# Kernel tuning notes

Measured on AMD Instinct MI355X. Metric: run time of the kernel, lower is better.

Reference implementation:

```python
import jax, jax.numpy as jnp
import numpy as np

# ---- layer config (yolov3, layer_no=2) ----
STRIDE = 8
N_CLASSES = 80
IGNORE_TH = 0.7
ANCHORS_PX = np.array([[10,13],[16,30],[33,23],[30,61],[62,45],[59,119],[116,90],[156,198],[373,326]], np.float32)
ALL_ANCHORS = ANCHORS_PX / STRIDE          # [9,2] in grid units
ANCHOR_ID_LO, ANCHOR_ID_HI = 0, 2          # anchor_mask[2] = [0,1,2]
ANCHORS = ALL_ANCHORS[ANCHOR_ID_LO:ANCHOR_ID_HI+1]  # [3,2]
NA = 3
NC = N_CLASSES + 5

B, IN_CH, NG, NBOX = 16, 256, 76, 50


def _safe_log(p):
    # emulate torch BCE's log clamp at -100; eps stops 0*inf -> nan
    return jnp.maximum(jnp.log(jnp.maximum(p, 1e-12)), -100.0)


def _bce_sum(p, t, w=None):
    l = -(t * _safe_log(p) + (1.0 - t) * _safe_log(1.0 - p))
    if w is not None:
        l = l * w
    return l.sum()


def setup_inputs() -> dict:
    key = jax.random.key(0)
    k1, k2, k3, k4, k5 = jax.random.split(key, 5)
    xin = jax.random.normal(k1, (B, IN_CH, NG, NG), jnp.float32)
    cls = jax.random.randint(k2, (B, NBOX, 1), 0, N_CLASSES).astype(jnp.float32)
    cxy = jax.random.uniform(k3, (B, NBOX, 2), jnp.float32, 0.02, 0.98)
    wh = jax.random.uniform(k4, (B, NBOX, 2), jnp.float32, 0.02, 0.40)
    labels = jnp.concatenate([cls, cxy, wh], axis=-1)  # [B,N,5]
    W = jax.random.normal(k5, (NA * NC, IN_CH), jnp.float32) * 0.02  # 1x1 conv
    b = jnp.zeros((NA * NC,), jnp.float32)
    return {"xin": xin, "labels": labels, "W": W, "b": b}


def _yolo_loss(xin, labels, W, b):
    nB, _, nG, _ = xin.shape
    anchors = jnp.asarray(ANCHORS, xin.dtype)          # [3,2]
    all_anchors = jnp.asarray(ALL_ANCHORS, xin.dtype)  # [9,2]

    # 1x1 conv -> [B, A, G, G, C]
    x = jnp.einsum('bchw,oc->bohw', xin, W) + b[None, :, None, None]
    x = x.reshape(nB, NA, NC, nG, nG).transpose(0, 1, 3, 4, 2)

    xy = jax.nn.sigmoid(x[..., :2])
    wh = x[..., 2:4]
    conf_cls = jax.nn.sigmoid(x[..., 4:])  # [B,A,G,G,1+ncls]

    gy, gx = jnp.meshgrid(jnp.arange(nG, dtype=x.dtype), jnp.arange(nG, dtype=x.dtype), indexing='ij')
    pred_boxes = jnp.stack([
        xy[..., 0] + gx,
        xy[..., 1] + gy,
        jnp.exp(wh[..., 0]) * anchors[:, 0][None, :, None, None],
        jnp.exp(wh[..., 1]) * anchors[:, 1][None, :, None, None]], axis=-1)  # [B,A,G,G,4]

    # ---- ground truth ----
    valid = labels.sum(-1) > 0                     # [B,N]
    gt_cls = labels[..., 0].astype(jnp.int32)
    gt = labels[..., 1:] * nG                      # [B,N,4] cx,cy,w,h in grid units
    gt_x, gt_y, gt_w, gt_h = gt[..., 0], gt[..., 1], gt[..., 2], gt[..., 3]
    gi = jnp.floor(gt_x).astype(jnp.int32)
    gj = jnp.floor(gt_y).astype(jnp.int32)

    # best anchor per gt: wh-IoU vs all 9 anchors (centered at origin)
    inter_a = jnp.minimum(gt_w[..., None], all_anchors[:, 0]) * jnp.minimum(gt_h[..., None], all_anchors[:, 1])
    union_a = gt_w[..., None] * gt_h[..., None] + all_anchors[:, 0] * all_anchors[:, 1] - inter_a
    best = jnp.argmax(inter_a / union_a, axis=-1)  # [B,N]
    in_mask = (best >= ANCHOR_ID_LO) & (best <= ANCHOR_ID_HI)
    a = jnp.where(in_mask, best % 3, -1)           # [B,N]

    # all-pairs IoU: pred boxes vs gt boxes (ignore mask)
    pb = pred_boxes.reshape(nB, -1, 4)             # [B,M,4], M = A*G*G
    pa_area = pb[..., 2] * pb[..., 3]
    gt_area = gt_w * gt_h
    tl = jnp.maximum(pb[:, :, None, :2] - pb[:, :, None, 2:] / 2, gt[:, None, :, :2] - gt[:, None, :, 2:] / 2)
    br = jnp.minimum(pb[:, :, None, :2] + pb[:, :, None, 2:] / 2, gt[:, None, :, :2] + gt[:, None, :, 2:] / 2)
    inter = jnp.prod(br - tl, -1) * jnp.all(tl < br, -1)
    iou = inter / (pa_area[:, :, None] + gt_area[:, None, :] - inter)
    iou = jnp.where(valid[:, None, :], iou, 0.0)
    best_iou = iou.max(-1)                         # [B,M]
    has_boxes = valid.any(-1)
    obj_mask = jnp.where(has_boxes[:, None], best_iou <= IGNORE_TH, True).reshape(nB, NA, nG, nG)

    # ---- scatter target assignment ----
    assign = valid & (a >= 0)
    a_safe = jnp.clip(a, 0, NA - 1)
    aw = anchors[a_safe, 0]
    ah = anchors[a_safe, 1]
    tvec = jnp.concatenate([
        (gt_x - jnp.floor(gt_x))[..., None],
        (gt_y - jnp.floor(gt_y))[..., None],
        jnp.log(gt_w / aw + 1e-16)[..., None],
        jnp.log(gt_h / ah + 1e-16)[..., None],
        jnp.ones_like(gt_x)[..., None],
        jax.nn.one_hot(gt_cls, N_CLASSES, dtype=x.dtype)], axis=-1)  # [B,N,NC]
    sval = 2.0 - gt_w * gt_h / (nG * nG)

    bf = jnp.broadcast_to(jnp.arange(nB)[:, None], a.shape).reshape(-1)
    af = jnp.where(assign, a_safe, NA).reshape(-1)  # NA is OOB -> dropped
    jf = gj.reshape(-1)
    if_ = gi.reshape(-1)

    target = jnp.zeros((nB, NA, nG, nG, NC), x.dtype).at[bf, af, jf, if_].set(tvec.reshape(-1, NC), mode='drop')
    scale = jnp.zeros((nB, NA, nG, nG), x.dtype).at[bf, af, jf, if_].set(sval.reshape(-1), mode='drop')
    obj_mask = obj_mask.at[bf, af, jf, if_].set(True, mode='drop')
    noobj = jnp.zeros((nB, NA, nG, nG), bool).at[bf, af, jf, if_].set(True, mode='drop')

    # ---- losses ----
    nm = noobj.astype(x.dtype)[..., None]
    p_obj = conf_cls[..., 0] * obj_mask
    t_obj = target[..., 4] * obj_mask
    p_xy = xy * nm
    t_xy = target[..., :2] * nm
    p_wh = wh * nm
    t_wh = target[..., 2:4] * nm
    p_cls = conf_cls[..., 1:] * nm
    t_cls = target[..., 5:] * nm
    sc = scale[..., None]

    loss_xy = _bce_sum(p_xy, t_xy, sc)
    rs = jnp.sqrt(sc)
    loss_wh = 0.5 * jnp.sum((p_wh * rs - t_wh * rs) ** 2)
    loss_obj = _bce_sum(p_obj, t_obj)
    loss_cls = _bce_sum(p_cls, t_cls)
    loss = loss_xy + loss_wh + loss_obj + loss_cls
    return jnp.stack([loss, loss_xy, loss_wh, loss_obj, loss_cls])


def reference(xin, labels, W, b):
    return _yolo_loss(xin, labels, W, b)
```

## Files before the change

kernel.cpp:

```cpp
#include <hip/hip_runtime.h>
#include <math.h>

#define NB    16
#define NAg   3
#define NCg   85
#define NCLS  80
#define NGg   76
#define NSp   (NGg*NGg)
#define NBOX  50
#define INCH  256
#define SPB   256

#define ACC_OFF  0
#define HAS_OFF  32
#define WT_OFF   128
#define GB_OFF   (WT_OFF + 16384)
#define GA_OFF   (GB_OFF + 25600)
#define GI_OFF   (GA_OFF + 25600)

__device__ __constant__ float c_AW[9] = {1.25f,2.0f,4.125f,3.75f,7.75f,7.375f,14.5f,19.5f,46.625f};
__device__ __constant__ float c_AH[9] = {1.625f,3.75f,2.875f,7.625f,5.625f,14.875f,11.25f,24.75f,40.75f};

__device__ __forceinline__ float safe_log(float p) {
    return fmaxf(logf(fmaxf(p, 1e-12f)), -100.0f);
}
__device__ __forceinline__ float sigm(float x) {
    return 1.0f / (1.0f + expf(-x));
}

__global__ __launch_bounds__(256) void k_labels(
    const float* __restrict__ labels, const float* __restrict__ W,
    float* __restrict__ Wt, float* __restrict__ gbox, float* __restrict__ gaux,
    int* __restrict__ gint, int* __restrict__ hasAny, float* __restrict__ acc)
{
    const int b = blockIdx.x, tid = threadIdx.x;
    const int t = b * 256 + tid;

    {
        const int c = t >> 4, f = t & 15;
        Wt[t] = (f < 15) ? W[((f / 5) * NCg + (f % 5)) * INCH + c] : 0.f;
    }
    if (b == 0 && tid < 8) acc[tid] = 0.f;

    int valid = 0;
    if (tid < NBOX) {
        const int bt = b * NBOX + tid;
        const float* L = labels + (size_t)bt * 5;
        const float l0 = L[0], l1 = L[1], l2 = L[2], l3 = L[3], l4 = L[4];
        valid = (l0 + l1 + l2 + l3 + l4) > 0.f;

        const float gx = l1 * NGg, gy = l2 * NGg, gw = l3 * NGg, gh = l4 * NGg;

        int best = 0; float brr = -1.f;
#pragma unroll
        for (int k = 0; k < 9; k++) {
            float inter = fminf(gw, c_AW[k]) * fminf(gh, c_AH[k]);
            float uni   = gw*gh + c_AW[k]*c_AH[k] - inter;
            float r     = inter / uni;
            if (r > brr) { brr = r; best = k; }
        }
        const int a = (best <= 2) ? best : -1;
        const int assign = valid && (a >= 0);
        const int a_safe = a < 0 ? 0 : (a > 2 ? 2 : a);

        const int gi = (int)floorf(gx), gj = (int)floorf(gy);
        const int inb = (gi >= 0) && (gi < NGg) && (gj >= 0) && (gj < NGg);
        const int cell = (assign && inb) ? (a * NSp + gj * NGg + gi) : -1;

        float* gb = gbox + (size_t)bt * 8;
        gb[0] = gx - gw * 0.5f;
        gb[1] = gy - gh * 0.5f;
        gb[2] = gx + gw * 0.5f;
        gb[3] = gy + gh * 0.5f;
        gb[4] = valid ? gw * gh : -1.f;
        gb[5] = __int_as_float(cell);

        float* ga = gaux + (size_t)bt * 8;
        ga[0] = gx - floorf(gx);
        ga[1] = gy - floorf(gy);
        ga[2] = logf(gw / c_AW[a_safe] + 1e-16f);
        ga[3] = logf(gh / c_AH[a_safe] + 1e-16f);
        ga[4] = 2.f - gw * gh / (float)NSp;

        gint[bt*2 + 0] = cell;
        gint[bt*2 + 1] = (int)l0;
    }
    if (tid < 64) {
        const unsigned long long m = __ballot(valid != 0);
        if (tid == 0) hasAny[b] = (m != 0ULL) ? 1 : 0;
    }
}

__global__ __launch_bounds__(256) void k_main(
    const float* __restrict__ xin, const float* __restrict__ Wt,
    const float* __restrict__ bias, const float* __restrict__ gbox,
    const int* __restrict__ hasAny, float* __restrict__ acc)
{
    __shared__ float part[4][15][SPB];
    __shared__ float wred[4];

    const int b   = blockIdx.y;
    const int tid = threadIdx.x;
    const int w   = tid >> 6, l = tid & 63;
    const int wu  = __builtin_amdgcn_readfirstlane(w);
    const int pb  = blockIdx.x * SPB;

    float4 ac[15];
#pragma unroll
    for (int f = 0; f < 15; ++f) ac[f] = make_float4(0.f,0.f,0.f,0.f);

    const float* xp = xin + ((size_t)b * INCH + (wu << 6)) * NSp + pb + 4*l;
    const float* wp = Wt + ((wu << 6) << 4);

    if (pb + SPB <= NSp) {
        for (int c0 = 0; c0 < 64; c0 += 8) {
            float4 v[8];
#pragma unroll
            for (int k = 0; k < 8; ++k)
                v[k] = *(const float4*)(xp + (size_t)(c0 + k) * NSp);
#pragma unroll
            for (int k = 0; k < 8; ++k) {
                const float* wr = wp + ((c0 + k) << 4);
#pragma unroll
                for (int f = 0; f < 15; ++f) {
                    const float wv = wr[f];
                    ac[f].x += wv * v[k].x;  ac[f].y += wv * v[k].y;
                    ac[f].z += wv * v[k].z;  ac[f].w += wv * v[k].w;
                }
            }
        }
    } else {
        const bool lv = (pb + 4*l) < NSp;
        const float4 z = make_float4(0.f,0.f,0.f,0.f);
        for (int c0 = 0; c0 < 64; c0 += 8) {
            float4 v[8];
#pragma unroll
            for (int k = 0; k < 8; ++k)
                v[k] = lv ? *(const float4*)(xp + (size_t)(c0 + k) * NSp) : z;
#pragma unroll
            for (int k = 0; k < 8; ++k) {
                const float* wr = wp + ((c0 + k) << 4);
#pragma unroll
                for (int f = 0; f < 15; ++f) {
                    const float wv = wr[f];
                    ac[f].x += wv * v[k].x;  ac[f].y += wv * v[k].y;
                    ac[f].z += wv * v[k].z;  ac[f].w += wv * v[k].w;
                }
            }
        }
    }

#pragma unroll
    for (int f = 0; f < 15; ++f)
        *(float4*)&part[w][f][4*l] = ac[f];
    __syncthreads();

    float lsum = 0.f;
    const int p = pb + tid;
    if (p < NSp) {
        float xv[15];
#pragma unroll
        for (int f = 0; f < 15; ++f)
            xv[f] = part[0][f][tid] + part[1][f][tid]
                  + part[2][f][tid] + part[3][f][tid];

        const int sy = p / NGg;
        const int sx = p - sy * NGg;
        const float gxf = (float)sx, gyf = (float)sy;

        float pbx0[3], pby0[3], pbx1[3], pby1[3], pa[3], cf[3];
#pragma unroll
        for (int a = 0; a < 3; ++a) {
            const float px = sigm(xv[a*5+0] + bias[a*NCg+0]) + gxf;
            const float py = sigm(xv[a*5+1] + bias[a*NCg+1]) + gyf;
            const float pw = expf(xv[a*5+2] + bias[a*NCg+2]) * c_AW[a];
            const float ph = expf(xv[a*5+3] + bias[a*NCg+3]) * c_AH[a];
            cf[a]   = sigm(xv[a*5+4] + bias[a*NCg+4]);
            pbx0[a] = px - pw * 0.5f;  pby0[a] = py - ph * 0.5f;
            pbx1[a] = px + pw * 0.5f;  pby1[a] = py + ph * 0.5f;
            pa[a]   = pw * ph;
        }

        int mask = 0;
        const float* gb = gbox + (size_t)b * NBOX * 8;
        for (int n = 0; n < NBOX; ++n) {
            const float bx0 = gb[n*8+0], by0 = gb[n*8+1];
            const float bx1 = gb[n*8+2], by1 = gb[n*8+3];
            const float gar = gb[n*8+4];
            const int cell  = __float_as_int(gb[n*8+5]);
            const int d = cell - p;
            if (d == 0)       mask |= 8;
            if (d == NSp)     mask |= 16;
            if (d == 2*NSp)   mask |= 32;
            if (gar >= 0.f) {
#pragma unroll
                for (int a = 0; a < 3; ++a) {
                    const float tlx = fmaxf(pbx0[a], bx0);
                    const float tly = fmaxf(pby0[a], by0);
                    const float brx = fminf(pbx1[a], bx1);
                    const float bry = fminf(pby1[a], by1);
                    const float dx = brx - tlx, dy = bry - tly;
                    const float inter = (dx > 0.f && dy > 0.f) ? dx * dy : 0.f;
                    if (inter > 0.7f * (pa[a] + gar - inter)) mask |= (1 << a);
                }
            }
        }

        const bool hasB = hasAny[b] != 0;
#pragma unroll
        for (int a = 0; a < 3; ++a) {
            const bool ex = (mask & (1 << a)) != 0;
            const bool as = (mask & (8 << a)) != 0;
            const bool maskpre = hasB ? (!ex) : true;
            if (maskpre || as) {
                const float c = cf[a];
                lsum += as ? -safe_log(c) : -safe_log(1.f - c);
            }
        }
    }

#pragma unroll
    for (int off = 32; off > 0; off >>= 1) lsum += __shfl_down(lsum, off);
    if (l == 0) wred[w] = lsum;
    __syncthreads();
    if (tid == 0) atomicAdd(&acc[2], wred[0] + wred[1] + wred[2] + wred[3]);
}

__global__ __launch_bounds__(256) void k_assigned(
    const float* __restrict__ xin, const float* __restrict__ W,
    const float* __restrict__ bias, const float* __restrict__ gaux,
    const int* __restrict__ gint, float* __restrict__ acc)
{
    const int t = blockIdx.x;
    const int b = t / NBOX, n = t % NBOX;
    const int tid = threadIdx.x;

    __shared__ int   scell[NBOX];
    __shared__ float4 col4[64];
    __shared__ float  xsh[NCg];
    __shared__ float  sacc[3];

    if (tid < NBOX) scell[tid] = gint[(b * NBOX + tid) * 2];
    __syncthreads();

    const int cell = scell[n];
    if (cell < 0) return;
    for (int n2 = n + 1; n2 < NBOX; ++n2)
        if (scell[n2] == cell) return;

    const int a = cell / NSp, s = cell % NSp;
    const int o0 = a * NCg;

    ((float*)col4)[tid] = xin[((size_t)b * INCH + tid) * NSp + s];
    if (tid < 3) sacc[tid] = 0.f;
    __syncthreads();

    const int wid = tid >> 6, lane = tid & 63;
    for (int o = wid; o < NCg; o += 4) {
        const float4 wv = *(const float4*)&W[(size_t)(o0 + o) * INCH + lane * 4];
        const float4 cv = col4[lane];
        float p = wv.x*cv.x + wv.y*cv.y + wv.z*cv.z + wv.w*cv.w;
        for (int off = 32; off; off >>= 1) p += __shfl_down(p, off);
        if (lane == 0) xsh[o] = p + bias[o0 + o];
    }
    __syncthreads();

    if (tid < NCg) {
        const float* ga = gaux + (size_t)t * 8;
        const float sval = ga[4];
        const int gcls = gint[t*2 + 1];
        float val = xsh[tid];
        float term; int slot;
        if (tid < 2) {
            float tgt = ga[tid];
            float p = sigm(val);
            term = -(tgt * safe_log(p) + (1.f - tgt) * safe_log(1.f - p)) * sval;
            slot = 0;
        } else if (tid < 4) {
            float tgt = ga[tid];
            float d = val - tgt;
            term = 0.5f * sval * d * d;
            slot = 1;
        } else if (tid == 4) {
            term = 0.f; slot = 2;
        } else {
            float tgt = ((tid - 5) == gcls) ? 1.f : 0.f;
            float p = sigm(val);
            term = -(tgt * safe_log(p) + (1.f - tgt) * safe_log(1.f - p));
            slot = 2;
        }
        atomicAdd(&sacc[slot], term);
    }
    __syncthreads();
    if (tid == 0) {
        atomicAdd(&acc[0], sacc[0]);
        atomicAdd(&acc[1], sacc[1]);
        atomicAdd(&acc[3], sacc[2]);
    }
}

__global__ void k_final(const float* __restrict__ acc, float* __restrict__ out)
{
    float xy = acc[0], wh = acc[1], ob = acc[2], cl = acc[3];
    out[0] = xy + wh + ob + cl;
    out[1] = xy; out[2] = wh; out[3] = ob; out[4] = cl;
}

extern "C" void kernel_launch(void* const* d_in, const int* in_sizes, int n_in,
                              void* d_out, int out_size, void* d_ws, size_t ws_size,
                              hipStream_t stream)
{
    const float* xin    = (const float*)d_in[0];
    const float* labels = (const float*)d_in[1];
    const float* W      = (const float*)d_in[2];
    const float* bias   = (const float*)d_in[3];

    char* ws = (char*)d_ws;
    float* acc    = (float*)(ws + ACC_OFF);
    int*   hasAny = (int*)  (ws + HAS_OFF);
    float* Wt     = (float*)(ws + WT_OFF);
    float* gbox   = (float*)(ws + GB_OFF);
    float* gaux   = (float*)(ws + GA_OFF);
    int*   gint   = (int*)  (ws + GI_OFF);
    float* out    = (float*)d_out;

    k_labels<<<16, 256, 0, stream>>>(labels, W, Wt, gbox, gaux, gint, hasAny, acc);

    k_main<<<dim3((NSp + SPB - 1) / SPB, NB), 256, 0, stream>>>(xin, Wt, bias, gbox, hasAny, acc);

    k_assigned<<<dim3(NB * NBOX), 256, 0, stream>>>(xin, W, bias, gaux, gint, acc);

    k_final<<<1, 1, 0, stream>>>(acc, out);
}
```

Baseline: 194.7 us.

## Merge main, assigned-cell and final kernels into one launch with last-block finish

Folds the per-cell objectness kernel, the assigned-box kernel and the final reduction kernel into a single launch. Extra blocks along x handle the assigned boxes, and a global done counter lets the last block write the output. This removes two kernel launches and their serialization gaps. In exchange it adds a shared-memory union, an atomic counter with a fence per block, and extra barriers on the assigned path.

Result: slower. 205.2 us (+5.4%).

```diff
diff --git a/kernel.cpp b/kernel.cpp
--- a/kernel.cpp
+++ b/kernel.cpp
@@ -10,9 +10,13 @@
 #define NBOX  50
 #define INCH  256
 #define SPB   256
+#define GBLK  ((NSp + SPB - 1) / SPB)
+#define GXDIM (GBLK + NBOX)
+#define TOTBLK (GXDIM * NB)
 
 #define ACC_OFF  0
 #define HAS_OFF  32
+#define DONE_OFF 96
 #define WT_OFF   128
 #define GB_OFF   (WT_OFF + 16384)
 #define GA_OFF   (GB_OFF + 25600)
@@ -31,7 +35,8 @@
 __global__ __launch_bounds__(256) void k_labels(
     const float* __restrict__ labels, const float* __restrict__ W,
     float* __restrict__ Wt, float* __restrict__ gbox, float* __restrict__ gaux,
-    int* __restrict__ gint, int* __restrict__ hasAny, float* __restrict__ acc)
+    int* __restrict__ gint, int* __restrict__ hasAny, float* __restrict__ acc,
+    int* __restrict__ done)
 {
     const int b = blockIdx.x, tid = threadIdx.x;
     const int t = b * 256 + tid;
@@ -40,7 +45,8 @@
         const int c = t >> 4, f = t & 15;
         Wt[t] = (f < 15) ? W[((f / 5) * NCg + (f % 5)) * INCH + c] : 0.f;
     }
-    if (b == 0 && tid < 8) acc[tid] = 0.f;
+    if (b == 0 && tid < 8)  acc[tid] = 0.f;
+    if (b == 0 && tid == 8) *done = 0;
 
     int valid = 0;
     if (tid < NBOX) {
@@ -91,219 +97,231 @@
     }
 }
 
-__global__ __launch_bounds__(256) void k_main(
+__global__ __launch_bounds__(256) void k_mega(
     const float* __restrict__ xin, const float* __restrict__ Wt,
-    const float* __restrict__ bias, const float* __restrict__ gbox,
-    const int* __restrict__ hasAny, float* __restrict__ acc)
+    const float* __restrict__ W, const float* __restrict__ bias,
+    const float* __restrict__ gbox, const float* __restrict__ gaux,
+    const int* __restrict__ gint, const int* __restrict__ hasAny,
+    float* __restrict__ acc, int* __restrict__ done, float* __restrict__ out)
 {
-    __shared__ float part[4][15][SPB];
-    __shared__ float wred[4];
-
+    __shared__ __align__(16) float smem[15364];
+
+    const int bx  = blockIdx.x;
     const int b   = blockIdx.y;
     const int tid = threadIdx.x;
-    const int w   = tid >> 6, l = tid & 63;
-    const int wu  = __builtin_amdgcn_readfirstlane(w);
-    const int pb  = blockIdx.x * SPB;
-
-    float4 ac[15];
-#pragma unroll
-    for (int f = 0; f < 15; ++f) ac[f] = make_float4(0.f,0.f,0.f,0.f);
-
-    const float* xp = xin + ((size_t)b * INCH + (wu << 6)) * NSp + pb + 4*l;
-    const float* wp = Wt + ((wu << 6) << 4);
-
-    if (pb + SPB <= NSp) {
-        for (int c0 = 0; c0 < 64; c0 += 8) {
-            float4 v[8];
-#pragma unroll
-            for (int k = 0; k < 8; ++k)
-                v[k] = *(const float4*)(xp + (size_t)(c0 + k) * NSp);
-#pragma unroll
-            for (int k = 0; k < 8; ++k) {
-                const float* wr = wp + ((c0 + k) << 4);
-#pragma unroll
-                for (int f = 0; f < 15; ++f) {
-                    const float wv = wr[f];
-                    ac[f].x += wv * v[k].x;  ac[f].y += wv * v[k].y;
-                    ac[f].z += wv * v[k].z;  ac[f].w += wv * v[k].w;
-                }
-            }
-        }
+
+    if (bx < GBLK) {
+        float (*part)[15][SPB] = (float (*)[15][SPB])smem;
+        float* wred = smem + 4 * 15 * SPB;
+
+        const int w  = tid >> 6, l = tid & 63;
+        const int wu = __builtin_amdgcn_readfirstlane(w);
+        const int pb = bx * SPB;
+
+        float4 ac[15];
+#pragma unroll
+        for (int f = 0; f < 15; ++f) ac[f] = make_float4(0.f,0.f,0.f,0.f);
+
+        const float* xp = xin + ((size_t)b * INCH + (wu << 6)) * NSp + pb + 4*l;
+        const float* wp = Wt + ((wu << 6) << 4);
+
+        if (pb + SPB <= NSp) {
+            for (int c0 = 0; c0 < 64; c0 += 8) {
+                float4 v[8];
+#pragma unroll
+                for (int k = 0; k < 8; ++k)
+                    v[k] = *(const float4*)(xp + (size_t)(c0 + k) * NSp);
+#pragma unroll
+                for (int k = 0; k < 8; ++k) {
+                    const float* wr = wp + ((c0 + k) << 4);
+#pragma unroll
+                    for (int f = 0; f < 15; ++f) {
+                        const float wv = wr[f];
+                        ac[f].x += wv * v[k].x;  ac[f].y += wv * v[k].y;
+                        ac[f].z += wv * v[k].z;  ac[f].w += wv * v[k].w;
+                    }
+                }
+            }
+        } else {
+            const bool lv = (pb + 4*l) < NSp;
+            const float4 z = make_float4(0.f,0.f,0.f,0.f);
+            for (int c0 = 0; c0 < 64; c0 += 8) {
+                float4 v[8];
+#pragma unroll
+                for (int k = 0; k < 8; ++k)
+                    v[k] = lv ? *(const float4*)(xp + (size_t)(c0 + k) * NSp) : z;
+#pragma unroll
+                for (int k = 0; k < 8; ++k) {
+                    const float* wr = wp + ((c0 + k) << 4);
+#pragma unroll
+                    for (int f = 0; f < 15; ++f) {
+                        const float wv = wr[f];
+                        ac[f].x += wv * v[k].x;  ac[f].y += wv * v[k].y;
+                        ac[f].z += wv * v[k].z;  ac[f].w += wv * v[k].w;
+                    }
+                }
+            }
+        }
+
+#pragma unroll
+        for (int f = 0; f < 15; ++f)
+            *(float4*)&part[w][f][4*l] = ac[f];
+        __syncthreads();
+
+        float lsum = 0.f;
+        const int p = pb + tid;
+        if (p < NSp) {
+            float xv[15];
+#pragma unroll
+            for (int f = 0; f < 15; ++f)
+                xv[f] = part[0][f][tid] + part[1][f][tid]
+                      + part[2][f][tid] + part[3][f][tid];
+
+            const int sy = p / NGg;
+            const int sx = p - sy * NGg;
+            const float gxf = (float)sx, gyf = (float)sy;
+
+            float pbx0[3], pby0[3], pbx1[3], pby1[3], pa[3], cf[3];
+#pragma unroll
+            for (int a = 0; a < 3; ++a) {
+                const float px = sigm(xv[a*5+0] + bias[a*NCg+0]) + gxf;
+                const float py = sigm(xv[a*5+1] + bias[a*NCg+1]) + gyf;
+                const float pw = expf(xv[a*5+2] + bias[a*NCg+2]) * c_AW[a];
+                const float ph = expf(xv[a*5+3] + bias[a*NCg+3]) * c_AH[a];
+                cf[a]   = sigm(xv[a*5+4] + bias[a*NCg+4]);
+                pbx0[a] = px - pw * 0.5f;  pby0[a] = py - ph * 0.5f;
+                pbx1[a] = px + pw * 0.5f;  pby1[a] = py + ph * 0.5f;
+                pa[a]   = pw * ph;
+            }
+
+            int mask = 0;
+            const float* gb = gbox + (size_t)b * NBOX * 8;
+            for (int n = 0; n < NBOX; ++n) {
+                const float bx0 = gb[n*8+0], by0 = gb[n*8+1];
+                const float bx1 = gb[n*8+2], by1 = gb[n*8+3];
+                const float gar = gb[n*8+4];
+                const int cell  = __float_as_int(gb[n*8+5]);
+                const int d = cell - p;
+                if (d == 0)       mask |= 8;
+                if (d == NSp)     mask |= 16;
+                if (d == 2*NSp)   mask |= 32;
+                if (gar >= 0.f) {
+#pragma unroll
+                    for (int a = 0; a < 3; ++a) {
+                        const float tlx = fmaxf(pbx0[a], bx0);
+                        const float tly = fmaxf(pby0[a], by0);
+                        const float brx = fminf(pbx1[a], bx1);
+                        const float bry = fminf(pby1[a], by1);
+                        const float dx = brx - tlx, dy = bry - tly;
+                        const float inter = (dx > 0.f && dy > 0.f) ? dx * dy : 0.f;
+                        if (inter > 0.7f * (pa[a] + gar - inter)) mask |= (1 << a);
+                    }
+                }
+            }
+
+            const bool hasB = hasAny[b] != 0;
+#pragma unroll
+            for (int a = 0; a < 3; ++a) {
+                const bool ex = (mask & (1 << a)) != 0;
+                const bool as = (mask & (8 << a)) != 0;
+                const bool maskpre = hasB ? (!ex) : true;
+                if (maskpre || as) {
+                    const float c = cf[a];
+                    lsum += as ? -safe_log(c) : -safe_log(1.f - c);
+                }
+            }
+        }
+
+#pragma unroll
+        for (int off = 32; off > 0; off >>= 1) lsum += __shfl_down(lsum, off);
+        if ((tid & 63) == 0) wred[tid >> 6] = lsum;
+        __syncthreads();
+        if (tid == 0) atomicAdd(&acc[2], wred[0] + wred[1] + wred[2] + wred[3]);
+
     } else {
-        const bool lv = (pb + 4*l) < NSp;
-        const float4 z = make_float4(0.f,0.f,0.f,0.f);
-        for (int c0 = 0; c0 < 64; c0 += 8) {
-            float4 v[8];
-#pragma unroll
-            for (int k = 0; k < 8; ++k)
-                v[k] = lv ? *(const float4*)(xp + (size_t)(c0 + k) * NSp) : z;
-#pragma unroll
-            for (int k = 0; k < 8; ++k) {
-                const float* wr = wp + ((c0 + k) << 4);
-#pragma unroll
-                for (int f = 0; f < 15; ++f) {
-                    const float wv = wr[f];
-                    ac[f].x += wv * v[k].x;  ac[f].y += wv * v[k].y;
-                    ac[f].z += wv * v[k].z;  ac[f].w += wv * v[k].w;
-                }
-            }
-        }
-    }
-
-#pragma unroll
-    for (int f = 0; f < 15; ++f)
-        *(float4*)&part[w][f][4*l] = ac[f];
-    __syncthreads();
-
-    float lsum = 0.f;
-    const int p = pb + tid;
-    if (p < NSp) {
-        float xv[15];
-#pragma unroll
-        for (int f = 0; f < 15; ++f)
-            xv[f] = part[0][f][tid] + part[1][f][tid]
-                  + part[2][f][tid] + part[3][f][tid];
-
-        const int sy = p / NGg;
-        const int sx = p - sy * NGg;
-        const float gxf = (float)sx, gyf = (float)sy;
-
-        float pbx0[3], pby0[3], pbx1[3], pby1[3], pa[3], cf[3];
-#pragma unroll
-        for (int a = 0; a < 3; ++a) {
-            const float px = sigm(xv[a*5+0] + bias[a*NCg+0]) + gxf;
-            const float py = sigm(xv[a*5+1] + bias[a*NCg+1]) + gyf;
-            const float pw = expf(xv[a*5+2] + bias[a*NCg+2]) * c_AW[a];
-            const float ph = expf(xv[a*5+3] + bias[a*NCg+3]) * c_AH[a];
-            cf[a]   = sigm(xv[a*5+4] + bias[a*NCg+4]);
-            pbx0[a] = px - pw * 0.5f;  pby0[a] = py - ph * 0.5f;
-            pbx1[a] = px + pw * 0.5f;  pby1[a] = py + ph * 0.5f;
-            pa[a]   = pw * ph;
-        }
-
-        int mask = 0;
-        const float* gb = gbox + (size_t)b * NBOX * 8;
-        for (int n = 0; n < NBOX; ++n) {
-            const float bx0 = gb[n*8+0], by0 = gb[n*8+1];
-            const float bx1 = gb[n*8+2], by1 = gb[n*8+3];
-            const float gar = gb[n*8+4];
-            const int cell  = __float_as_int(gb[n*8+5]);
-            const int d = cell - p;
-            if (d == 0)       mask |= 8;
-            if (d == NSp)     mask |= 16;
-            if (d == 2*NSp)   mask |= 32;
-            if (gar >= 0.f) {
-#pragma unroll
-                for (int a = 0; a < 3; ++a) {
-                    const float tlx = fmaxf(pbx0[a], bx0);
-                    const float tly = fmaxf(pby0[a], by0);
-                    const float brx = fminf(pbx1[a], bx1);
-                    const float bry = fminf(pby1[a], by1);
-                    const float dx = brx - tlx, dy = bry - tly;
-                    const float inter = (dx > 0.f && dy > 0.f) ? dx * dy : 0.f;
-                    if (inter > 0.7f * (pa[a] + gar - inter)) mask |= (1 << a);
-                }
-            }
-        }
-
-        const bool hasB = hasAny[b] != 0;
-#pragma unroll
-        for (int a = 0; a < 3; ++a) {
-            const bool ex = (mask & (1 << a)) != 0;
-            const bool as = (mask & (8 << a)) != 0;
-            const bool maskpre = hasB ? (!ex) : true;
-            if (maskpre || as) {
-                const float c = cf[a];
-                lsum += as ? -safe_log(c) : -safe_log(1.f - c);
-            }
-        }
-    }
-
-#pragma unroll
-    for (int off = 32; off > 0; off >>= 1) lsum += __shfl_down(lsum, off);
-    if (l == 0) wred[w] = lsum;
-    __syncthreads();
-    if (tid == 0) atomicAdd(&acc[2], wred[0] + wred[1] + wred[2] + wred[3]);
-}
-
-__global__ __launch_bounds__(256) void k_assigned(
-    const float* __restrict__ xin, const float* __restrict__ W,
-    const float* __restrict__ bias, const float* __restrict__ gaux,
-    const int* __restrict__ gint, float* __restrict__ acc)
-{
-    const int t = blockIdx.x;
-    const int b = t / NBOX, n = t % NBOX;
-    const int tid = threadIdx.x;
-
-    __shared__ int   scell[NBOX];
-    __shared__ float4 col4[64];
-    __shared__ float  xsh[NCg];
-    __shared__ float  sacc[3];
-
-    if (tid < NBOX) scell[tid] = gint[(b * NBOX + tid) * 2];
-    __syncthreads();
-
-    const int cell = scell[n];
-    if (cell < 0) return;
-    for (int n2 = n + 1; n2 < NBOX; ++n2)
-        if (scell[n2] == cell) return;
-
-    const int a = cell / NSp, s = cell % NSp;
-    const int o0 = a * NCg;
-
-    ((float*)col4)[tid] = xin[((size_t)b * INCH + tid) * NSp + s];
-    if (tid < 3) sacc[tid] = 0.f;
-    __syncthreads();
-
-    const int wid = tid >> 6, lane = tid & 63;
-    for (int o = wid; o < NCg; o += 4) {
-        const float4 wv = *(const float4*)&W[(size_t)(o0 + o) * INCH + lane * 4];
-        const float4 cv = col4[lane];
-        float p = wv.x*cv.x + wv.y*cv.y + wv.z*cv.z + wv.w*cv.w;
-        for (int off = 32; off; off >>= 1) p += __shfl_down(p, off);
-        if (lane == 0) xsh[o] = p + bias[o0 + o];
-    }
-    __syncthreads();
-
-    if (tid < NCg) {
-        const float* ga = gaux + (size_t)t * 8;
-        const float sval = ga[4];
-        const int gcls = gint[t*2 + 1];
-        float val = xsh[tid];
-        float term; int slot;
-        if (tid < 2) {
-            float tgt = ga[tid];
-            float p = sigm(val);
-            term = -(tgt * safe_log(p) + (1.f - tgt) * safe_log(1.f - p)) * sval;
-            slot = 0;
-        } else if (tid < 4) {
-            float tgt = ga[tid];
-            float d = val - tgt;
-            term = 0.5f * sval * d * d;
-            slot = 1;
-        } else if (tid == 4) {
-            term = 0.f; slot = 2;
-        } else {
-            float tgt = ((tid - 5) == gcls) ? 1.f : 0.f;
-            float p = sigm(val);
-            term = -(tgt * safe_log(p) + (1.f - tgt) * safe_log(1.f - p));
-            slot = 2;
-        }
-        atomicAdd(&sacc[slot], term);
-    }
+        int*    scell = (int*)smem;
+        float4* col4  = (float4*)(smem + 64);
+        float*  xsh   = smem + 64 + 256;
+        float*  sacc  = smem + 64 + 256 + 96;
+
+        const int n = bx - GBLK;
+        const int t = b * NBOX + n;
+
+        if (tid < NBOX) scell[tid] = gint[(b * NBOX + tid) * 2];
+        __syncthreads();
+
+        const int cell = scell[n];
+        bool win = (cell >= 0);
+        if (win)
+            for (int n2 = n + 1; n2 < NBOX; ++n2)
+                if (scell[n2] == cell) { win = false; break; }
+
+        if (win) {
+            const int a = cell / NSp, s = cell % NSp;
+            const int o0 = a * NCg;
+
+            ((float*)col4)[tid] = xin[((size_t)b * INCH + tid) * NSp + s];
+            if (tid < 3) sacc[tid] = 0.f;
+            __syncthreads();
+
+            const int wid = tid >> 6, lane = tid & 63;
+            for (int o = wid; o < NCg; o += 4) {
+                const float4 wv = *(const float4*)&W[(size_t)(o0 + o) * INCH + lane * 4];
+                const float4 cv = col4[lane];
+                float p = wv.x*cv.x + wv.y*cv.y + wv.z*cv.z + wv.w*cv.w;
+                for (int off = 32; off; off >>= 1) p += __shfl_down(p, off);
+                if (lane == 0) xsh[o] = p + bias[o0 + o];
+            }
+            __syncthreads();
+
+            if (tid < NCg) {
+                const float* ga = gaux + (size_t)t * 8;
+                const float sval = ga[4];
+                const int gcls = gint[t*2 + 1];
+                float val = xsh[tid];
+                float term; int slot;
+                if (tid < 2) {
+                    float tgt = ga[tid];
+                    float p = sigm(val);
+                    term = -(tgt * safe_log(p) + (1.f - tgt) * safe_log(1.f - p)) * sval;
+                    slot = 0;
+                } else if (tid < 4) {
+                    float tgt = ga[tid];
+                    float d = val - tgt;
+                    term = 0.5f * sval * d * d;
+                    slot = 1;
+                } else if (tid == 4) {
+                    term = 0.f; slot = 2;
+                } else {
+                    float tgt = ((tid - 5) == gcls) ? 1.f : 0.f;
+                    float p = sigm(val);
+                    term = -(tgt * safe_log(p) + (1.f - tgt) * safe_log(1.f - p));
+                    slot = 2;
+                }
+                atomicAdd(&sacc[slot], term);
+            }
+            __syncthreads();
+            if (tid == 0) {
+                atomicAdd(&acc[0], sacc[0]);
+                atomicAdd(&acc[1], sacc[1]);
+                atomicAdd(&acc[3], sacc[2]);
+            }
+        }
+    }
+
     __syncthreads();
     if (tid == 0) {
-        atomicAdd(&acc[0], sacc[0]);
-        atomicAdd(&acc[1], sacc[1]);
-        atomicAdd(&acc[3], sacc[2]);
-    }
-}
-
-__global__ void k_final(const float* __restrict__ acc, float* __restrict__ out)
-{
-    float xy = acc[0], wh = acc[1], ob = acc[2], cl = acc[3];
-    out[0] = xy + wh + ob + cl;
-    out[1] = xy; out[2] = wh; out[3] = ob; out[4] = cl;
+        __threadfence();
+        const int v = atomicAdd(done, 1);
+        if (v == TOTBLK - 1) {
+            const float xy = atomicAdd(&acc[0], 0.f);
+            const float wh = atomicAdd(&acc[1], 0.f);
+            const float ob = atomicAdd(&acc[2], 0.f);
+            const float cl = atomicAdd(&acc[3], 0.f);
+            out[0] = xy + wh + ob + cl;
+            out[1] = xy; out[2] = wh; out[3] = ob; out[4] = cl;
+        }
+    }
 }
 
 extern "C" void kernel_launch(void* const* d_in, const int* in_sizes, int n_in,
@@ -318,17 +336,15 @@
     char* ws = (char*)d_ws;
     float* acc    = (float*)(ws + ACC_OFF);
     int*   hasAny = (int*)  (ws + HAS_OFF);
+    int*   done   = (int*)  (ws + DONE_OFF);
     float* Wt     = (float*)(ws + WT_OFF);
     float* gbox   = (float*)(ws + GB_OFF);
     float* gaux   = (float*)(ws + GA_OFF);
     int*   gint   = (int*)  (ws + GI_OFF);
     float* out    = (float*)d_out;
 
-    k_labels<<<16, 256, 0, stream>>>(labels, W, Wt, gbox, gaux, gint, hasAny, acc);
-
-    k_main<<<dim3((NSp + SPB - 1) / SPB, NB), 256, 0, stream>>>(xin, Wt, bias, gbox, hasAny, acc);
-
-    k_assigned<<<dim3(NB * NBOX), 256, 0, stream>>>(xin, W, bias, gaux, gint, acc);
-
-    k_final<<<1, 1, 0, stream>>>(acc, out);
-}
+    k_labels<<<16, 256, 0, stream>>>(labels, W, Wt, gbox, gaux, gint, hasAny, acc, done);
+
+    k_mega<<<dim3(GXDIM, NB), 256, 0, stream>>>(xin, Wt, W, bias, gbox, gaux,
+                                                gint, hasAny, acc, done, out);
+}
```

## Give each thread four pixels over all channels and fold final reduction into last block

Applied to the files above, without the earlier changes.

k_main now has each thread accumulate all 256 input channels for four consecutive pixels and run the IoU/objectness loss on all four itself. This removes the per-wave channel split and its shared-memory partial-sum reduction and barrier. The separate k_final launch is replaced by a done-counter, so whichever block finishes last writes the output. k_assigned now runs before k_main. The grid shrinks to 6x16 blocks with a long serial channel loop per thread, which risks poor occupancy and latency hiding on a large GPU.

After: 313.6 us. 61.1% more time.

```diff
diff --git a/kernel.cpp b/kernel.cpp
--- a/kernel.cpp
+++ b/kernel.cpp
@@ -9,10 +9,13 @@
 #define NSp   (NGg*NGg)
 #define NBOX  50
 #define INCH  256
-#define SPB   256
+#define SPB   1024
+#define GBLK  ((NSp + SPB - 1) / SPB)
+#define TOTALL (GBLK * NB + NB * NBOX)
 
 #define ACC_OFF  0
 #define HAS_OFF  32
+#define DONE_OFF 96
 #define WT_OFF   128
 #define GB_OFF   (WT_OFF + 16384)
 #define GA_OFF   (GB_OFF + 25600)
@@ -31,7 +34,8 @@
 __global__ __launch_bounds__(256) void k_labels(
     const float* __restrict__ labels, const float* __restrict__ W,
     float* __restrict__ Wt, float* __restrict__ gbox, float* __restrict__ gaux,
-    int* __restrict__ gint, int* __restrict__ hasAny, float* __restrict__ acc)
+    int* __restrict__ gint, int* __restrict__ hasAny, float* __restrict__ acc,
+    int* __restrict__ done)
 {
     const int b = blockIdx.x, tid = threadIdx.x;
     const int t = b * 256 + tid;
@@ -40,7 +44,8 @@
         const int c = t >> 4, f = t & 15;
         Wt[t] = (f < 15) ? W[((f / 5) * NCg + (f % 5)) * INCH + c] : 0.f;
     }
-    if (b == 0 && tid < 8) acc[tid] = 0.f;
+    if (b == 0 && tid < 8)  acc[tid] = 0.f;
+    if (b == 0 && tid == 8) *done = 0;
 
     int valid = 0;
     if (tid < NBOX) {
@@ -91,130 +96,196 @@
     }
 }
 
+__global__ __launch_bounds__(256) void k_assigned(
+    const float* __restrict__ xin, const float* __restrict__ W,
+    const float* __restrict__ bias, const float* __restrict__ gaux,
+    const int* __restrict__ gint, float* __restrict__ acc,
+    int* __restrict__ done, float* __restrict__ out)
+{
+    const int t = blockIdx.x;
+    const int b = t / NBOX, n = t % NBOX;
+    const int tid = threadIdx.x;
+
+    __shared__ int   scell[NBOX];
+    __shared__ float4 col4[64];
+    __shared__ float  xsh[NCg];
+    __shared__ float  sacc[3];
+
+    if (tid < NBOX) scell[tid] = gint[(b * NBOX + tid) * 2];
+    __syncthreads();
+
+    const int cell = scell[n];
+    bool win = (cell >= 0);
+    if (win)
+        for (int n2 = n + 1; n2 < NBOX; ++n2)
+            if (scell[n2] == cell) { win = false; break; }
+
+    if (win) {
+        const int a = cell / NSp, s = cell % NSp;
+        const int o0 = a * NCg;
+
+        ((float*)col4)[tid] = xin[((size_t)b * INCH + tid) * NSp + s];
+        if (tid < 3) sacc[tid] = 0.f;
+        __syncthreads();
+
+        const int wid = tid >> 6, lane = tid & 63;
+        for (int o = wid; o < NCg; o += 4) {
+            const float4 wv = *(const float4*)&W[(size_t)(o0 + o) * INCH + lane * 4];
+            const float4 cv = col4[lane];
+            float p = wv.x*cv.x + wv.y*cv.y + wv.z*cv.z + wv.w*cv.w;
+            for (int off = 32; off; off >>= 1) p += __shfl_down(p, off);
+            if (lane == 0) xsh[o] = p + bias[o0 + o];
+        }
+        __syncthreads();
+
+        if (tid < NCg) {
+            const float* ga = gaux + (size_t)t * 8;
+            const float sval = ga[4];
+            const int gcls = gint[t*2 + 1];
+            float val = xsh[tid];
+            float term; int slot;
+            if (tid < 2) {
+                float tgt = ga[tid];
+                float p = sigm(val);
+                term = -(tgt * safe_log(p) + (1.f - tgt) * safe_log(1.f - p)) * sval;
+                slot = 0;
+            } else if (tid < 4) {
+                float tgt = ga[tid];
+                float d = val - tgt;
+                term = 0.5f * sval * d * d;
+                slot = 1;
+            } else if (tid == 4) {
+                term = 0.f; slot = 2;
+            } else {
+                float tgt = ((tid - 5) == gcls) ? 1.f : 0.f;
+                float p = sigm(val);
+                term = -(tgt * safe_log(p) + (1.f - tgt) * safe_log(1.f - p));
+                slot = 2;
+            }
+            atomicAdd(&sacc[slot], term);
+        }
+        __syncthreads();
+        if (tid == 0) {
+            atomicAdd(&acc[0], sacc[0]);
+            atomicAdd(&acc[1], sacc[1]);
+            atomicAdd(&acc[3], sacc[2]);
+        }
+    }
+
+    if (tid == 0) {
+        __threadfence();
+        const int v = atomicAdd(done, 1);
+        if (v == TOTALL - 1) {
+            const float xy = atomicAdd(&acc[0], 0.f);
+            const float wh = atomicAdd(&acc[1], 0.f);
+            const float ob = atomicAdd(&acc[2], 0.f);
+            const float cl = atomicAdd(&acc[3], 0.f);
+            out[0] = xy + wh + ob + cl;
+            out[1] = xy; out[2] = wh; out[3] = ob; out[4] = cl;
+        }
+    }
+}
+
 __global__ __launch_bounds__(256) void k_main(
     const float* __restrict__ xin, const float* __restrict__ Wt,
     const float* __restrict__ bias, const float* __restrict__ gbox,
-    const int* __restrict__ hasAny, float* __restrict__ acc)
+    const int* __restrict__ hasAny, float* __restrict__ acc,
+    int* __restrict__ done, float* __restrict__ out)
 {
-    __shared__ float part[4][15][SPB];
     __shared__ float wred[4];
 
+    const int bx  = blockIdx.x;
     const int b   = blockIdx.y;
     const int tid = threadIdx.x;
     const int w   = tid >> 6, l = tid & 63;
-    const int wu  = __builtin_amdgcn_readfirstlane(w);
-    const int pb  = blockIdx.x * SPB;
+    const int pb  = bx * SPB;
+    const bool live = (pb + 4*tid) < NSp;
 
     float4 ac[15];
 #pragma unroll
     for (int f = 0; f < 15; ++f) ac[f] = make_float4(0.f,0.f,0.f,0.f);
 
-    const float* xp = xin + ((size_t)b * INCH + (wu << 6)) * NSp + pb + 4*l;
-    const float* wp = Wt + ((wu << 6) << 4);
-
-    if (pb + SPB <= NSp) {
-        for (int c0 = 0; c0 < 64; c0 += 8) {
-            float4 v[8];
-#pragma unroll
-            for (int k = 0; k < 8; ++k)
-                v[k] = *(const float4*)(xp + (size_t)(c0 + k) * NSp);
-#pragma unroll
-            for (int k = 0; k < 8; ++k) {
-                const float* wr = wp + ((c0 + k) << 4);
-#pragma unroll
-                for (int f = 0; f < 15; ++f) {
-                    const float wv = wr[f];
-                    ac[f].x += wv * v[k].x;  ac[f].y += wv * v[k].y;
-                    ac[f].z += wv * v[k].z;  ac[f].w += wv * v[k].w;
+    const float* xp = xin + (size_t)b * INCH * NSp + pb + 4*tid;
+    const float4 z = make_float4(0.f,0.f,0.f,0.f);
+
+    for (int c0 = 0; c0 < INCH; c0 += 8) {
+        float4 v[8];
+#pragma unroll
+        for (int k = 0; k < 8; ++k)
+            v[k] = live ? *(const float4*)(xp + (size_t)(c0 + k) * NSp) : z;
+#pragma unroll
+        for (int k = 0; k < 8; ++k) {
+            const float* wr = Wt + ((c0 + k) << 4);
+#pragma unroll
+            for (int f = 0; f < 15; ++f) {
+                const float wv = wr[f];
+                ac[f].x += wv * v[k].x;  ac[f].y += wv * v[k].y;
+                ac[f].z += wv * v[k].z;  ac[f].w += wv * v[k].w;
+            }
+        }
+    }
+
+    float lsum = 0.f;
+    if (live) {
+        const bool hasB = hasAny[b] != 0;
+        const float* gb = gbox + (size_t)b * NBOX * 8;
+#pragma unroll
+        for (int q = 0; q < 4; ++q) {
+            const int p = pb + 4*tid + q;
+            float xv[15];
+#pragma unroll
+            for (int f = 0; f < 15; ++f) xv[f] = ((const float*)&ac[f])[q];
+
+            const int sy = p / NGg;
+            const int sx = p - sy * NGg;
+            const float gxf = (float)sx, gyf = (float)sy;
+
+            float pbx0[3], pby0[3], pbx1[3], pby1[3], pa[3], cf[3];
+#pragma unroll
+            for (int a = 0; a < 3; ++a) {
+                const float px = sigm(xv[a*5+0] + bias[a*NCg+0]) + gxf;
+                const float py = sigm(xv[a*5+1] + bias[a*NCg+1]) + gyf;
+                const float pw = expf(xv[a*5+2] + bias[a*NCg+2]) * c_AW[a];
+                const float ph = expf(xv[a*5+3] + bias[a*NCg+3]) * c_AH[a];
+                cf[a]   = sigm(xv[a*5+4] + bias[a*NCg+4]);
+                pbx0[a] = px - pw * 0.5f;  pby0[a] = py - ph * 0.5f;
+                pbx1[a] = px + pw * 0.5f;  pby1[a] = py + ph * 0.5f;
+                pa[a]   = pw * ph;
+            }
+
+            int mask = 0;
+            for (int n = 0; n < NBOX; ++n) {
+                const float bx0 = gb[n*8+0], by0 = gb[n*8+1];
+                const float bx1 = gb[n*8+2], by1 = gb[n*8+3];
+                const float gar = gb[n*8+4];
+                const int cell  = __float_as_int(gb[n*8+5]);
+                const int d = cell - p;
+                if (d == 0)       mask |= 8;
+                if (d == NSp)     mask |= 16;
+                if (d == 2*NSp)   mask |= 32;
+                if (gar >= 0.f) {
+#pragma unroll
+                    for (int a = 0; a < 3; ++a) {
+                        const float tlx = fmaxf(pbx0[a], bx0);
+                        const float tly = fmaxf(pby0[a], by0);
+                        const float brx = fminf(pbx1[a], bx1);
+                        const float bry = fminf(pby1[a], by1);
+                        const float dx = brx - tlx, dy = bry - tly;
+                        const float inter = (dx > 0.f && dy > 0.f) ? dx * dy : 0.f;
+                        if (inter > 0.7f * (pa[a] + gar - inter)) mask |= (1 << a);
+                    }
                 }
             }
-        }
-    } else {
-        const bool lv = (pb + 4*l) < NSp;
-        const float4 z = make_float4(0.f,0.f,0.f,0.f);
-        for (int c0 = 0; c0 < 64; c0 += 8) {
-            float4 v[8];
-#pragma unroll
-            for (int k = 0; k < 8; ++k)
-                v[k] = lv ? *(const float4*)(xp + (size_t)(c0 + k) * NSp) : z;
-#pragma unroll
-            for (int k = 0; k < 8; ++k) {
-                const float* wr = wp + ((c0 + k) << 4);
-#pragma unroll
-                for (int f = 0; f < 15; ++f) {
-                    const float wv = wr[f];
-                    ac[f].x += wv * v[k].x;  ac[f].y += wv * v[k].y;
-                    ac[f].z += wv * v[k].z;  ac[f].w += wv * v[k].w;
+
+#pragma unroll
+            for (int a = 0; a < 3; ++a) {
+                const bool ex = (mask & (1 << a)) != 0;
+                const bool as = (mask & (8 << a)) != 0;
+                const bool maskpre = hasB ? (!ex) : true;
+                if (maskpre || as) {
+                    const float c = cf[a];
+                    lsum += as ? -safe_log(c) : -safe_log(1.f - c);
                 }
-            }
-        }
-    }
-
-#pragma unroll
-    for (int f = 0; f < 15; ++f)
-        *(float4*)&part[w][f][4*l] = ac[f];
-    __syncthreads();
-
-    float lsum = 0.f;
-    const int p = pb + tid;
-    if (p < NSp) {
-        float xv[15];
-#pragma unroll
-        for (int f = 0; f < 15; ++f)
-            xv[f] = part[0][f][tid] + part[1][f][tid]
-                  + part[2][f][tid] + part[3][f][tid];
-
-        const int sy = p / NGg;
-        const int sx = p - sy * NGg;
-        const float gxf = (float)sx, gyf = (float)sy;
-
-        float pbx0[3], pby0[3], pbx1[3], pby1[3], pa[3], cf[3];
-#pragma unroll
-        for (int a = 0; a < 3; ++a) {
-            const float px = sigm(xv[a*5+0] + bias[a*NCg+0]) + gxf;
-            const float py = sigm(xv[a*5+1] + bias[a*NCg+1]) + gyf;
-            const float pw = expf(xv[a*5+2] + bias[a*NCg+2]) * c_AW[a];
-            const float ph = expf(xv[a*5+3] + bias[a*NCg+3]) * c_AH[a];
-            cf[a]   = sigm(xv[a*5+4] + bias[a*NCg+4]);
-            pbx0[a] = px - pw * 0.5f;  pby0[a] = py - ph * 0.5f;
-            pbx1[a] = px + pw * 0.5f;  pby1[a] = py + ph * 0.5f;
-            pa[a]   = pw * ph;
-        }
-
-        int mask = 0;
-        const float* gb = gbox + (size_t)b * NBOX * 8;
-        for (int n = 0; n < NBOX; ++n) {
-            const float bx0 = gb[n*8+0], by0 = gb[n*8+1];
-            const float bx1 = gb[n*8+2], by1 = gb[n*8+3];
-            const float gar = gb[n*8+4];
-            const int cell  = __float_as_int(gb[n*8+5]);
-            const int d = cell - p;
-            if (d == 0)       mask |= 8;
-            if (d == NSp)     mask |= 16;
-            if (d == 2*NSp)   mask |= 32;
-            if (gar >= 0.f) {
-#pragma unroll
-                for (int a = 0; a < 3; ++a) {
-                    const float tlx = fmaxf(pbx0[a], bx0);
-                    const float tly = fmaxf(pby0[a], by0);
-                    const float brx = fminf(pbx1[a], bx1);
-                    const float bry = fminf(pby1[a], by1);
-                    const float dx = brx - tlx, dy = bry - tly;
-                    const float inter = (dx > 0.f && dy > 0.f) ? dx * dy : 0.f;
-                    if (inter > 0.7f * (pa[a] + gar - inter)) mask |= (1 << a);
-                }
-            }
-        }
-
-        const bool hasB = hasAny[b] != 0;
-#pragma unroll
-        for (int a = 0; a < 3; ++a) {
-            const bool ex = (mask & (1 << a)) != 0;
-            const bool as = (mask & (8 << a)) != 0;
-            const bool maskpre = hasB ? (!ex) : true;
-            if (maskpre || as) {
-                const float c = cf[a];
-                lsum += as ? -safe_log(c) : -safe_log(1.f - c);
             }
         }
     }
@@ -224,86 +295,19 @@
     if (l == 0) wred[w] = lsum;
     __syncthreads();
     if (tid == 0) atomicAdd(&acc[2], wred[0] + wred[1] + wred[2] + wred[3]);
-}
-
-__global__ __launch_bounds__(256) void k_assigned(
-    const float* __restrict__ xin, const float* __restrict__ W,
-    const float* __restrict__ bias, const float* __restrict__ gaux,
-    const int* __restrict__ gint, float* __restrict__ acc)
-{
-    const int t = blockIdx.x;
-    const int b = t / NBOX, n = t % NBOX;
-    const int tid = threadIdx.x;
-
-    __shared__ int   scell[NBOX];
-    __shared__ float4 col4[64];
-    __shared__ float  xsh[NCg];
-    __shared__ float  sacc[3];
-
-    if (tid < NBOX) scell[tid] = gint[(b * NBOX + tid) * 2];
-    __syncthreads();
-
-    const int cell = scell[n];
-    if (cell < 0) return;
-    for (int n2 = n + 1; n2 < NBOX; ++n2)
-        if (scell[n2] == cell) return;
-
-    const int a = cell / NSp, s = cell % NSp;
-    const int o0 = a * NCg;
-
-    ((float*)col4)[tid] = xin[((size_t)b * INCH + tid) * NSp + s];
-    if (tid < 3) sacc[tid] = 0.f;
-    __syncthreads();
-
-    const int wid = tid >> 6, lane = tid & 63;
-    for (int o = wid; o < NCg; o += 4) {
-        const float4 wv = *(const float4*)&W[(size_t)(o0 + o) * INCH + lane * 4];
-        const float4 cv = col4[lane];
-        float p = wv.x*cv.x + wv.y*cv.y + wv.z*cv.z + wv.w*cv.w;
-        for (int off = 32; off; off >>= 1) p += __shfl_down(p, off);
-        if (lane == 0) xsh[o] = p + bias[o0 + o];
-    }
-    __syncthreads();
-
-    if (tid < NCg) {
-        const float* ga = gaux + (size_t)t * 8;
-        const float sval = ga[4];
-        const int gcls = gint[t*2 + 1];
-        float val = xsh[tid];
-        float term; int slot;
-        if (tid < 2) {
-            float tgt = ga[tid];
-            float p = sigm(val);
-            term = -(tgt * safe_log(p) + (1.f - tgt) * safe_log(1.f - p)) * sval;
-            slot = 0;
-        } else if (tid < 4) {
-            float tgt = ga[tid];
-            float d = val - tgt;
-            term = 0.5f * sval * d * d;
-            slot = 1;
-        } else if (tid == 4) {
-            term = 0.f; slot = 2;
-        } else {
-            float tgt = ((tid - 5) == gcls) ? 1.f : 0.f;
-            float p = sigm(val);
-            term = -(tgt * safe_log(p) + (1.f - tgt) * safe_log(1.f - p));
-            slot = 2;
-        }
-        atomicAdd(&sacc[slot], term);
-    }
-    __syncthreads();
+
     if (tid == 0) {
-        atomicAdd(&acc[0], sacc[0]);
-        atomicAdd(&acc[1], sacc[1]);
-        atomicAdd(&acc[3], sacc[2]);
-    }
-}
-
-__global__ void k_final(const float* __restrict__ acc, float* __restrict__ out)
-{
-    float xy = acc[0], wh = acc[1], ob = acc[2], cl = acc[3];
-    out[0] = xy + wh + ob + cl;
-    out[1] = xy; out[2] = wh; out[3] = ob; out[4] = cl;
+        __threadfence();
+        const int v = atomicAdd(done, 1);
+        if (v == TOTALL - 1) {
+            const float xy = atomicAdd(&acc[0], 0.f);
+            const float wh = atomicAdd(&acc[1], 0.f);
+            const float ob = atomicAdd(&acc[2], 0.f);
+            const float cl = atomicAdd(&acc[3], 0.f);
+            out[0] = xy + wh + ob + cl;
+            out[1] = xy; out[2] = wh; out[3] = ob; out[4] = cl;
+        }
+    }
 }
 
 extern "C" void kernel_launch(void* const* d_in, const int* in_sizes, int n_in,
@@ -318,17 +322,18 @@
     char* ws = (char*)d_ws;
     float* acc    = (float*)(ws + ACC_OFF);
     int*   hasAny = (int*)  (ws + HAS_OFF);
+    int*   done   = (int*)  (ws + DONE_OFF);
     float* Wt     = (float*)(ws + WT_OFF);
     float* gbox   = (float*)(ws + GB_OFF);
     float* gaux   = (float*)(ws + GA_OFF);
     int*   gint   = (int*)  (ws + GI_OFF);
     float* out    = (float*)d_out;
 
-    k_labels<<<16, 256, 0, stream>>>(labels, W, Wt, gbox, gaux, gint, hasAny, acc);
-
-    k_main<<<dim3((NSp + SPB - 1) / SPB, NB), 256, 0, stream>>>(xin, Wt, bias, gbox, hasAny, acc);
-
-    k_assigned<<<dim3(NB * NBOX), 256, 0, stream>>>(xin, W, bias, gaux, gint, acc);
-
-    k_final<<<1, 1, 0, stream>>>(acc, out);
-}
+    k_labels<<<16, 256, 0, stream>>>(labels, W, Wt, gbox, gaux, gint, hasAny, acc, done);
+
+    k_assigned<<<dim3(NB * NBOX), 256, 0, stream>>>(xin, W, bias, gaux, gint,
+                                                    acc, done, out);
+
+    k_main<<<dim3(GBLK, NB), 256, 0, stream>>>(xin, Wt, bias, gbox, hasAny,
+                                               acc, done, out);
+}
```
